# Performance work log

Measured on AMD Instinct MI355X. Metric: run time of the kernel, lower is better.

Reference implementation:

```python
import jax, jax.numpy as jnp
import numpy as np

N_NODES = 100000
N_HYPEREDGES = 10000
NNZ = 1600000

def setup_inputs() -> dict:
    key = jax.random.key(0)
    k = jax.random.split(key, 7)
    return {
        "x": jax.random.normal(k[0], (N_NODES, 1), dtype=jnp.float32),
        "W1": jax.random.normal(k[1], (1, 128), dtype=jnp.float32) * 0.5,
        "b1": jax.random.normal(k[2], (128,), dtype=jnp.float32) * 0.1,
        "W2": jax.random.normal(k[3], (128, 1), dtype=jnp.float32) * 0.1,
        "b2": jax.random.normal(k[4], (1,), dtype=jnp.float32) * 0.1,
        "node_idx": jax.random.randint(k[5], (NNZ,), 0, N_NODES, dtype=jnp.int64),
        "edge_idx": jax.random.randint(k[6], (NNZ,), 0, N_HYPEREDGES, dtype=jnp.int64),
    }

def _hypergraph_conv(x, W, b, node_idx, edge_idx, n_nodes, n_edges):
    # PyG HypergraphConv (use_attention=False, hyperedge_weight=1):
    # out = D^-1 H B^-1 H^T (X W) + b
    x = x @ W  # [N, F_out]
    ones = jnp.ones(node_idx.shape[0], dtype=x.dtype)
    D = jax.ops.segment_sum(ones, node_idx, num_segments=n_nodes)   # node degree
    B = jax.ops.segment_sum(ones, edge_idx, num_segments=n_edges)   # hyperedge degree
    D_inv = jnp.where(D > 0, 1.0 / D, 0.0)
    B_inv = jnp.where(B > 0, 1.0 / B, 0.0)
    # node -> hyperedge: e = B^-1 H^T x
    e = B_inv[:, None] * jax.ops.segment_sum(x[node_idx], edge_idx, num_segments=n_edges)
    # hyperedge -> node: out = D^-1 H e
    out = D_inv[:, None] * jax.ops.segment_sum(e[edge_idx], node_idx, num_segments=n_nodes)
    return out + b

def reference(x, W1, b1, W2, b2, node_idx, edge_idx):
    n_nodes = x.shape[0]
    h = _hypergraph_conv(x, W1, b1, node_idx, edge_idx, n_nodes, N_HYPEREDGES)
    h = jax.nn.relu(h)
    out = _hypergraph_conv(h, W2, b2, node_idx, edge_idx, n_nodes, N_HYPEREDGES)
    return out
```

## Files before the change

kernel.cpp:

```cpp
#include <hip/hip_runtime.h>

static constexpr int N_NODES = 100000;
static constexpr int N_EDGES = 10000;
static constexpr int NNZ     = 1600000;

static constexpr int G1    = 256;
static constexpr int CHUNK = NNZ / G1;
static constexpr int NRN   = 250;
static constexpr int RN    = 400;
static constexpr int RE    = 40;
static constexpr int SLOT  = 64;
static constexpr int BLK   = 1024;
static constexpr int NW    = 16;
static constexpr int GF    = 250;
static constexpr int ITER  = G1 * SLOT / BLK;


__device__ __forceinline__ void st_a(float* p, float v) {
    __hip_atomic_store(p, v, __ATOMIC_RELAXED, __HIP_MEMORY_SCOPE_AGENT);
}

__device__ __forceinline__ void bar_arrive(unsigned* bar, int phase) {
    __syncthreads();
    if (threadIdx.x == 0)
        __hip_atomic_fetch_add(bar + phase * 256 + (blockIdx.x & 7) * 32, 1u,
                               __ATOMIC_RELAXED, __HIP_MEMORY_SCOPE_AGENT);
}
__device__ __forceinline__ void bar_wait(unsigned* bar, int phase) {
    if (threadIdx.x == 0) {
        unsigned* flag = bar + 768 + phase * 32;
        if (blockIdx.x == 0) {
            unsigned* cnt = bar + phase * 256;
            unsigned sum;
            do {
                __builtin_amdgcn_s_sleep(2);
                sum = 0u;
                #pragma unroll
                for (int g = 0; g < 8; ++g)
                    sum += __hip_atomic_load(cnt + g * 32, __ATOMIC_RELAXED,
                                             __HIP_MEMORY_SCOPE_AGENT);
            } while (sum < (unsigned)GF);
            __hip_atomic_store(flag, 1u, __ATOMIC_RELAXED, __HIP_MEMORY_SCOPE_AGENT);
        } else {
            while (__hip_atomic_load(flag, __ATOMIC_RELAXED,
                                     __HIP_MEMORY_SCOPE_AGENT) == 0u)
                __builtin_amdgcn_s_sleep(2);
        }
    }
    __syncthreads();
}

__global__ __launch_bounds__(BLK) void k_bin_agg(
        const int* __restrict__ nidx, const int* __restrict__ eidx,
        const float* __restrict__ x,
        unsigned* __restrict__ binN, unsigned* __restrict__ cntN,
        float* __restrict__ P_S1, unsigned* __restrict__ P_B1,
        unsigned* __restrict__ bar) {
    __shared__ float    sS[N_EDGES];
    __shared__ unsigned sC[N_EDGES / 2];
    __shared__ unsigned cN[NRN];
    if (blockIdx.x == 0 && threadIdx.x < 896) bar[threadIdx.x] = 0u;
    for (int j = threadIdx.x; j < N_EDGES; j += BLK) sS[j] = 0.0f;
    for (int j = threadIdx.x; j < N_EDGES / 2; j += BLK) sC[j] = 0u;
    for (int j = threadIdx.x; j < NRN; j += BLK) cN[j] = 0u;
    __syncthreads();
    const int b = blockIdx.x;
    const int i0 = b * CHUNK, i1 = i0 + CHUNK;
    for (int i = i0 + threadIdx.x; i < i1; i += BLK) {
        int n = nidx[i], e = eidx[i];
        atomicAdd(&sS[e], x[n]);
        atomicAdd(&sC[e >> 1], 1u << ((e & 1) * 16));
        int rn = n / RN;
        unsigned pn = atomicAdd(&cN[rn], 1u);
        binN[((size_t)rn * G1 + b) * SLOT + pn] = ((unsigned)(n - rn * RN) << 14) | (unsigned)e;
    }
    __syncthreads();
    for (int j = threadIdx.x; j < NRN; j += BLK) cntN[(size_t)j * G1 + b] = cN[j];
    float*    ps = P_S1 + (size_t)b * N_EDGES;
    unsigned* pb = P_B1 + (size_t)b * (N_EDGES / 2);
    for (int j = threadIdx.x; j < N_EDGES; j += BLK) ps[j] = sS[j];
    for (int j = threadIdx.x; j < N_EDGES / 2; j += BLK) pb[j] = sC[j];
}

__global__ __launch_bounds__(BLK) void k_fused(
        const unsigned* __restrict__ binN, const unsigned* __restrict__ cntN,
        const float* __restrict__ P_S1, const unsigned* __restrict__ P_B1,
        const float* __restrict__ W1, const float* __restrict__ b1,
        const float* __restrict__ W2, const float* __restrict__ b2,
        float* __restrict__ v1, float* __restrict__ v2, float* __restrict__ P_S,
        unsigned* __restrict__ bar, float* __restrict__ out) {
    __shared__ float    sBig[N_EDGES];
    __shared__ float    eS[NW][RE];
    __shared__ unsigned eC[NW][RE];
    __shared__ float    sS_n[RN];
    __shared__ unsigned sC_n[RN];
    __shared__ unsigned scntN[G1];
    __shared__ float    wgt[384];
    __shared__ float    y_loc[RN];

    const int b = blockIdx.x;
    const int t = threadIdx.x;
    const int wv = t >> 6;
    const int lane = t & 63;
    float my_binv = 0.0f;
    float my_dinv = 0.0f;

    if (lane < RE) {
        const int e = b * RE + lane;
        float s = 0.0f; unsigned c = 0u;
        for (int g = wv; g < G1; g += NW) {
            s += P_S1[(size_t)g * N_EDGES + e];
            c += (P_B1[(size_t)g * (N_EDGES / 2) + (e >> 1)] >> ((e & 1) * 16)) & 0xFFFFu;
        }
        eS[wv][lane] = s; eC[wv][lane] = c;
    }
    __syncthreads();
    if (t < RE) {
        float s = 0.0f; unsigned c = 0u;
        #pragma unroll
        for (int k = 0; k < NW; ++k) { s += eS[k][t]; c += eC[k][t]; }
        my_binv = (c > 0u) ? (1.0f / (float)c) : 0.0f;
        st_a(&v1[b * RE + t], s * my_binv);
    }
    bar_arrive(bar, 0);
    if (t < RN) { sS_n[t] = 0.0f; sC_n[t] = 0u; }
    if (t < G1) scntN[t] = cntN[(size_t)b * G1 + t];
    if (t < 128) { wgt[t] = W1[t]; wgt[128 + t] = b1[t]; wgt[256 + t] = W2[t]; }
    bar_wait(bar, 0);

    const unsigned* baseN = binN + (size_t)b * G1 * SLOT;
    for (int j = t; j < N_EDGES; j += BLK) sBig[j] = v1[j];
    __syncthreads();
    unsigned w_reg[ITER];
    #pragma unroll
    for (int it = 0; it < ITER; ++it) {
        const int j = t + it * BLK;
        const int s = j & (SLOT - 1), bb = j >> 6;
        unsigned w = 0xFFFFFFFFu;
        if ((unsigned)s < scntN[bb]) {
            w = baseN[j];
            atomicAdd(&sS_n[w >> 14], sBig[w & 0x3FFFu]);
            atomicAdd(&sC_n[w >> 14], 1u);
        }
        w_reg[it] = w;
    }
    __syncthreads();
    if (t < RN) {
        unsigned c = sC_n[t];
        my_dinv = (c > 0u) ? (1.0f / (float)c) : 0.0f;
        float tt = sS_n[t] * my_dinv;
        float acc = 0.0f;
        #pragma unroll
        for (int f = 0; f < 128; ++f) {
            float h = fmaf(tt, wgt[f], wgt[128 + f]);
            h = fmaxf(h, 0.0f);
            acc = fmaf(h, wgt[256 + f], acc);
        }
        y_loc[t] = acc;
    }
    __syncthreads();
    for (int j = t; j < N_EDGES; j += BLK) sBig[j] = 0.0f;
    __syncthreads();
    #pragma unroll
    for (int it = 0; it < ITER; ++it) {
        unsigned w = w_reg[it];
        if (w != 0xFFFFFFFFu) atomicAdd(&sBig[w & 0x3FFFu], y_loc[w >> 14]);
    }
    __syncthreads();
    {
        float* ps = P_S + (size_t)b * N_EDGES;
        for (int j = t; j < N_EDGES; j += BLK) st_a(&ps[j], sBig[j]);
    }
    bar_arrive(bar, 1);
    bar_wait(bar, 1);

    if (lane < RE) {
        float acc = 0.0f;
        for (int g = wv; g < GF; g += NW)
            acc += P_S[(size_t)g * N_EDGES + b * RE + lane];
        eS[wv][lane] = acc;
    }
    __syncthreads();
    if (t < RE) {
        float s = 0.0f;
        #pragma unroll
        for (int k = 0; k < NW; ++k) s += eS[k][t];
        st_a(&v2[b * RE + t], s * my_binv);
    }
    bar_arrive(bar, 2);
    if (t < RN) sS_n[t] = 0.0f;
    bar_wait(bar, 2);

    for (int j = t; j < N_EDGES; j += BLK) sBig[j] = v2[j];
    __syncthreads();
    #pragma unroll
    for (int it = 0; it < ITER; ++it) {
        unsigned w = w_reg[it];
        if (w != 0xFFFFFFFFu) atomicAdd(&sS_n[w >> 14], sBig[w & 0x3FFFu]);
    }
    __syncthreads();
    if (t < RN) out[b * RN + t] = fmaf(sS_n[t], my_dinv, b2[0]);
}

extern "C" void kernel_launch(void* const* d_in, const int* in_sizes, int n_in,
                              void* d_out, int out_size, void* d_ws, size_t ws_size,
                              hipStream_t stream) {
    const float* x    = (const float*)d_in[0];
    const float* W1   = (const float*)d_in[1];
    const float* b1   = (const float*)d_in[2];
    const float* W2   = (const float*)d_in[3];
    const float* b2   = (const float*)d_in[4];
    const int*   nidx = (const int*)d_in[5];
    const int*   eidx = (const int*)d_in[6];
    float*       out  = (float*)d_out;

    char* ws = (char*)d_ws;
    unsigned* binN = (unsigned*)(ws + 0);
    unsigned* cntN = (unsigned*)(ws + 16384000);
    float*    P_S1 = (float*)(ws + 16640000);
    unsigned* P_B1 = (unsigned*)(ws + 26880000);
    float*    v1   = (float*)(ws + 32000000);
    float*    v2   = (float*)(ws + 32040000);
    float*    P_S  = (float*)(ws + 32080000);
    unsigned* bar  = (unsigned*)(ws + 42080000);

    k_bin_agg<<<G1, BLK, 0, stream>>>(nidx, eidx, x, binN, cntN, P_S1, P_B1, bar);
    k_fused  <<<GF, BLK, 0, stream>>>(binN, cntN, P_S1, P_B1, W1, b1, W2, b2,
                                      v1, v2, P_S, bar, out);
}
```

Baseline: 75.34 us.

## Flatten partial-sum reductions across all lanes and overlap binning with barrier wait

The column reductions over per-block partials now use every thread, with flattened indexing and shared-memory atomics, instead of only 40 of 64 lanes per wave doing strided loops. The node-degree counting pass over the binned entries now runs before waiting on the first grid barrier, so it overlaps with other blocks finishing phase 0. The value-gather atomics move after the barrier into a second pass over the register-held entries. This adds an extra loop and more LDS atomic contention in exchange for more memory parallelism and less idle barrier time.

```diff
diff --git a/kernel.cpp b/kernel.cpp
--- a/kernel.cpp
+++ b/kernel.cpp
@@ -101,18 +101,26 @@
     const int b = blockIdx.x;
     const int t = threadIdx.x;
     const int wv = t >> 6;
-    const int lane = t & 63;
     float my_binv = 0.0f;
     float my_dinv = 0.0f;
 
-    if (lane < RE) {
-        const int e = b * RE + lane;
-        float s = 0.0f; unsigned c = 0u;
-        for (int g = wv; g < G1; g += NW) {
-            s += P_S1[(size_t)g * N_EDGES + e];
-            c += (P_B1[(size_t)g * (N_EDGES / 2) + (e >> 1)] >> ((e & 1) * 16)) & 0xFFFFu;
-        }
-        eS[wv][lane] = s; eC[wv][lane] = c;
+    for (int j = t; j < NW * RE; j += BLK) { (&eS[0][0])[j] = 0.0f; (&eC[0][0])[j] = 0u; }
+    __syncthreads();
+    {
+        const float* pv = P_S1 + (size_t)b * RE;
+        for (int j = t; j < G1 * RE; j += BLK) {
+            int g = j / RE;
+            int e = j - g * RE;
+            atomicAdd(&eS[wv][e], pv[(size_t)g * N_EDGES + e]);
+        }
+        const unsigned* pc = P_B1 + (size_t)b * (RE / 2);
+        for (int j = t; j < G1 * (RE / 2); j += BLK) {
+            int g = j / (RE / 2);
+            int k = j - g * (RE / 2);
+            unsigned c2 = pc[(size_t)g * (N_EDGES / 2) + k];
+            atomicAdd(&eC[wv][2 * k],     c2 & 0xFFFFu);
+            atomicAdd(&eC[wv][2 * k + 1], c2 >> 16);
+        }
     }
     __syncthreads();
     if (t < RE) {
@@ -123,14 +131,12 @@
         st_a(&v1[b * RE + t], s * my_binv);
     }
     bar_arrive(bar, 0);
+
     if (t < RN) { sS_n[t] = 0.0f; sC_n[t] = 0u; }
     if (t < G1) scntN[t] = cntN[(size_t)b * G1 + t];
     if (t < 128) { wgt[t] = W1[t]; wgt[128 + t] = b1[t]; wgt[256 + t] = W2[t]; }
-    bar_wait(bar, 0);
-
+    __syncthreads();
     const unsigned* baseN = binN + (size_t)b * G1 * SLOT;
-    for (int j = t; j < N_EDGES; j += BLK) sBig[j] = v1[j];
-    __syncthreads();
     unsigned w_reg[ITER];
     #pragma unroll
     for (int it = 0; it < ITER; ++it) {
@@ -139,7 +145,6 @@
         unsigned w = 0xFFFFFFFFu;
         if ((unsigned)s < scntN[bb]) {
             w = baseN[j];
-            atomicAdd(&sS_n[w >> 14], sBig[w & 0x3FFFu]);
             atomicAdd(&sC_n[w >> 14], 1u);
         }
         w_reg[it] = w;
@@ -148,6 +153,18 @@
     if (t < RN) {
         unsigned c = sC_n[t];
         my_dinv = (c > 0u) ? (1.0f / (float)c) : 0.0f;
+    }
+    bar_wait(bar, 0);
+
+    for (int j = t; j < N_EDGES; j += BLK) sBig[j] = v1[j];
+    __syncthreads();
+    #pragma unroll
+    for (int it = 0; it < ITER; ++it) {
+        unsigned w = w_reg[it];
+        if (w != 0xFFFFFFFFu) atomicAdd(&sS_n[w >> 14], sBig[w & 0x3FFFu]);
+    }
+    __syncthreads();
+    if (t < RN) {
         float tt = sS_n[t] * my_dinv;
         float acc = 0.0f;
         #pragma unroll
@@ -172,13 +189,16 @@
         for (int j = t; j < N_EDGES; j += BLK) st_a(&ps[j], sBig[j]);
     }
     bar_arrive(bar, 1);
+    for (int j = t; j < NW * RE; j += BLK) (&eS[0][0])[j] = 0.0f;
     bar_wait(bar, 1);
 
-    if (lane < RE) {
-        float acc = 0.0f;
-        for (int g = wv; g < GF; g += NW)
-            acc += P_S[(size_t)g * N_EDGES + b * RE + lane];
-        eS[wv][lane] = acc;
+    {
+        const float* pv = P_S + (size_t)b * RE;
+        for (int j = t; j < GF * RE; j += BLK) {
+            int g = j / RE;
+            int e = j - g * RE;
+            atomicAdd(&eS[wv][e], pv[(size_t)g * N_EDGES + e]);
+        }
     }
     __syncthreads();
     if (t < RE) {
```

New measurement: 95.67 us. 1.27x slower.
